# Optimization experiments

Measured on AMD Instinct MI355X. Metric: run time of the kernel, lower is better.

Reference implementation:

```python
import jax, jax.numpy as jnp
import numpy as np

BETA = 0.25
SCALE_NUM = 4  # len(latents_scale)


def setup_inputs() -> dict:
    key = jax.random.key(0)
    kz, ke = jax.random.split(key)
    z = jax.random.normal(kz, (8, 256, 32, 32), dtype=jnp.float32)
    emb_weight = jax.random.normal(ke, (16384, 256), dtype=jnp.float32) * 0.02
    return {"z": z, "emb_weight": emb_weight}


def reference(z, emb_weight):
    # z: [B, C, H, W] with C == vq_embed_dim and H == W (source reshapes with W twice)
    B, C, H, W = z.shape
    z_det = jax.lax.stop_gradient(z)

    # NOTE: in the source, `residual` is flattened ONCE before the scale loop and
    # never updated inside it, so every scale picks the same indices. We compute
    # the nearest-codebook assignment once (identical math, argmin of cdist is
    # invariant under sqrt, so squared distances suffice).
    residual = jnp.transpose(z_det, (0, 2, 3, 1)).reshape(-1, C)  # [N, D], N=B*H*W
    d2 = (jnp.sum(residual * residual, axis=1, keepdims=True)
          - 2.0 * residual @ emb_weight.T
          + jnp.sum(emb_weight * emb_weight, axis=1))  # [N, n_e]
    idx = jnp.argmin(d2, axis=1).reshape(B, W, W)  # [B, W, W]

    quantized = jnp.transpose(emb_weight[idx], (0, 3, 1, 2))  # [B, C, H, W]

    z_hat = jnp.zeros_like(z_det)
    loss = jnp.float32(0.0)
    for _ in range(SCALE_NUM):
        z_hat = z_hat + quantized
        loss = loss + BETA * jnp.mean((jax.lax.stop_gradient(z_hat) - z) ** 2) \
                    + jnp.mean((z_hat - z_det) ** 2)
    loss = loss / SCALE_NUM

    total_idx = jnp.concatenate([idx] * SCALE_NUM, axis=1)  # [B, SCALE_NUM*W, W]
    z_hat_out = z + jax.lax.stop_gradient(z_hat - z)  # straight-through
    return z_hat_out, loss, total_idx
```

## Files before the change

kernel.cpp:

```cpp
#include <hip/hip_runtime.h>

#define D      256
#define N_E    16384
#define NPTS   8192
#define ZOUT   2097152
#define MARGIN 2.0e-2f
#define STRIPS 4
#define ECH    17

typedef short bf16x8 __attribute__((ext_vector_type(8)));
typedef unsigned short us8 __attribute__((ext_vector_type(8)));
typedef float f32x16 __attribute__((ext_vector_type(16)));
typedef unsigned long long u64;

__device__ __forceinline__ unsigned short f2bf(float x) {
    unsigned int u = __float_as_uint(x);
    return (unsigned short)((u + 0x7FFFu + ((u >> 16) & 1u)) >> 16);
}
__device__ __forceinline__ float bf2f(unsigned short h) {
    return __uint_as_float((unsigned int)h << 16);
}
__device__ __forceinline__ void gl_lds16(const void* g, void* l) {
    __builtin_amdgcn_global_load_lds(
        (const __attribute__((address_space(1))) unsigned int*)g,
        (__attribute__((address_space(3))) unsigned int*)l, 16, 0, 0);
}

__global__ __launch_bounds__(256) void prep(
    const float* __restrict__ z, const float* __restrict__ emb,
    unsigned short* __restrict__ Zpk, float* __restrict__ Zf32,
    unsigned short* __restrict__ Epk, float* __restrict__ e2,
    float* __restrict__ loss) {
    __shared__ float sh[32];
    const int t = threadIdx.x;
    if (blockIdx.x == 0 && t == 0) loss[0] = 0.f;
    if (blockIdx.x < 256) {
        const int n0 = blockIdx.x * 32;
        const int p = t & 31, ks8 = t >> 5;
        const int n = n0 + p;
        const int b = n >> 10, hw = n & 1023;
        const float* zb = z + (size_t)b * 262144 + hw;
        const int k0 = ks8 * 32;
        float v[32];
        #pragma unroll
        for (int kk = 0; kk < 32; ++kk)
            v[kk] = zb[(size_t)(k0 + kk) * 1024];
        #pragma unroll
        for (int i = 0; i < 8; ++i) {
            float4 f = {v[i * 4], v[i * 4 + 1], v[i * 4 + 2], v[i * 4 + 3]};
            *(float4*)(Zf32 + (size_t)n * D + k0 + i * 4) = f;
        }
        const int g = n >> 5;
        #pragma unroll
        for (int i = 0; i < 4; ++i) {
            us8 hv;
            #pragma unroll
            for (int c = 0; c < 8; ++c) hv[c] = f2bf(-2.0f * v[i * 8 + c]);
            const int kabs = k0 + i * 8;
            const int ks = kabs >> 4;
            const int l = (n & 31) + ((kabs >> 3) & 1) * 32;
            *(us8*)(Zpk + ((size_t)(g * 16 + ks) * 64 + l) * 8) = hv;
        }
    } else {
        const int bi = blockIdx.x - 256;
        const int j0 = bi * 32;
        const int jj = j0 + (t >> 3), q = t & 7;
        const float* row = emb + (size_t)jj * D + q * 32;
        float v[32];
        float s = 0.f;
        #pragma unroll
        for (int i = 0; i < 8; ++i) {
            const float4 x = *(const float4*)(row + i * 4);
            v[i * 4] = x.x; v[i * 4 + 1] = x.y; v[i * 4 + 2] = x.z; v[i * 4 + 3] = x.w;
            s += x.x * x.x + x.y * x.y + x.z * x.z + x.w * x.w;
        }
        #pragma unroll
        for (int i = 0; i < 4; ++i) {
            us8 hv;
            #pragma unroll
            for (int c = 0; c < 8; ++c) hv[c] = f2bf(v[i * 8 + c]);
            const int kabs = q * 32 + i * 8;
            const int ks = kabs >> 4;
            const int l = (jj & 31) + ((kabs >> 3) & 1) * 32;
            *(us8*)(Epk + ((size_t)(bi * ECH + ks) * 64 + l) * 8) = hv;
        }
        s += __shfl_xor(s, 1);
        s += __shfl_xor(s, 2);
        s += __shfl_xor(s, 4);
        if (q == 0) { e2[jj] = s; sh[t >> 3] = s; }
        __syncthreads();
        if (t < 64) {
            us8 hv;
            #pragma unroll
            for (int c = 0; c < 8; ++c) hv[c] = 0;
            if (t < 32) {
                const float vv = sh[t];
                const unsigned short hi = f2bf(vv);
                hv[0] = hi;
                hv[1] = f2bf(vv - bf2f(hi));
            }
            *(us8*)(Epk + ((size_t)bi * ECH + 16) * 512 + t * 8) = hv;
        }
    }
}

__global__ __launch_bounds__(256, 1) void mfma_gemm(
    const unsigned short* __restrict__ Epk, const unsigned short* __restrict__ Zpk,
    float* __restrict__ tminv, u64* __restrict__ tmask) {
    __shared__ unsigned short Zbuf[64 * 512];

    const int tid = threadIdx.x, lane = tid & 63, wid = tid >> 6;
    const int c32 = lane & 31, l5 = lane >> 5;
    const int n0 = blockIdx.x * 128;
    const int cs0 = blockIdx.y * (STRIPS * 512);

    us8 puu;
    #pragma unroll
    for (int c = 0; c < 8; ++c) puu[c] = 0;
    if (l5 == 0) { puu[0] = 0x3F80; puu[1] = 0x3F80; }
    const bf16x8 pu = (bf16x8)puu;

    #pragma unroll
    for (int ks = 0; ks < 16; ++ks)
        gl_lds16(Zpk + ((size_t)((n0 >> 5) + wid) * 16 + ks) * 512 + lane * 8,
                 Zbuf + (wid * 16 + ks) * 512);
    __syncthreads();

    for (int s = 0; s < STRIPS; ++s) {
        const int cb = cs0 + s * 512 + wid * 128;
        const unsigned short* eb =
            Epk + ((size_t)(cb >> 5) * ECH) * 512 + lane * 8;
        const unsigned short* zb = Zbuf + lane * 8;

        f32x16 acc[4][4];
        const f32x16 z16 = {0.f};
        #pragma unroll
        for (int i = 0; i < 4; ++i)
            #pragma unroll
            for (int j = 0; j < 4; ++j) acc[i][j] = z16;

        bf16x8 eq0[4], eq1[4];
        #pragma unroll
        for (int f = 0; f < 4; ++f) {
            eq0[f] = *(const bf16x8*)(eb + (f * ECH + 0) * 512);
            eq1[f] = *(const bf16x8*)(eb + (f * ECH + 1) * 512);
        }
        bf16x8 pc[4], pn[4];
        #pragma unroll
        for (int j = 0; j < 4; ++j) pc[j] = *(const bf16x8*)(zb + (j * 16) * 512);

        #pragma unroll 2
        for (int ks = 0; ks < 16; ++ks) {
            bf16x8 ef[4];
            if ((ks & 1) == 0) {
                #pragma unroll
                for (int f = 0; f < 4; ++f) ef[f] = eq0[f];
            } else {
                #pragma unroll
                for (int f = 0; f < 4; ++f) ef[f] = eq1[f];
            }
            if (ks < 15) {
                if ((ks & 1) == 0) {
                    #pragma unroll
                    for (int f = 0; f < 4; ++f)
                        eq0[f] = *(const bf16x8*)(eb + (f * ECH + ks + 2) * 512);
                } else {
                    #pragma unroll
                    for (int f = 0; f < 4; ++f)
                        eq1[f] = *(const bf16x8*)(eb + (f * ECH + ks + 2) * 512);
                }
                #pragma unroll
                for (int j = 0; j < 4; ++j)
                    pn[j] = *(const bf16x8*)(zb + (j * 16 + ks + 1) * 512);
            }
            #pragma unroll
            for (int i = 0; i < 4; ++i)
                #pragma unroll
                for (int j = 0; j < 4; ++j)
                    acc[i][j] = __builtin_amdgcn_mfma_f32_32x32x16_bf16(
                        ef[i], pc[j], acc[i][j], 0, 0, 0);
            if (ks < 15) {
                #pragma unroll
                for (int j = 0; j < 4; ++j) pc[j] = pn[j];
            }
        }
        #pragma unroll
        for (int i = 0; i < 4; ++i)
            #pragma unroll
            for (int j = 0; j < 4; ++j)
                acc[i][j] = __builtin_amdgcn_mfma_f32_32x32x16_bf16(
                    eq0[i], pu, acc[i][j], 0, 0, 0);

        #pragma unroll
        for (int j = 0; j < 4; ++j) {
            #pragma unroll
            for (int gi = 0; gi < 2; ++gi) {
                float m = acc[2 * gi][j][0];
                #pragma unroll
                for (int r = 1; r < 16; ++r) m = fminf(m, acc[2 * gi][j][r]);
                #pragma unroll
                for (int r = 0; r < 16; ++r) m = fminf(m, acc[2 * gi + 1][j][r]);
                m = fminf(m, __shfl_xor(m, 32));
                const float th = m + MARGIN;
                unsigned mk[2];
                #pragma unroll
                for (int i = 0; i < 2; ++i) {
                    unsigned mm = 0;
                    #pragma unroll
                    for (int r = 0; r < 16; ++r) {
                        const int row = (r & 3) + 8 * (r >> 2) + 4 * l5;
                        mm |= (acc[2 * gi + i][j][r] <= th) ? (1u << row) : 0u;
                    }
                    mk[i] = mm | (unsigned)__shfl_xor((int)mm, 32);
                }
                if (l5 == 0) {
                    const size_t pt = (size_t)(n0 + j * 32 + c32);
                    const int g = (cb >> 6) + gi;
                    tminv[pt * 256 + g] = m;
                    tmask[pt * 256 + g] = ((u64)mk[1] << 32) | (u64)mk[0];
                }
            }
        }
    }
}

__global__ __launch_bounds__(1024) void rescore_quant(
    const float* __restrict__ tminv, const u64* __restrict__ tmask,
    const float* __restrict__ Zf32, const float* __restrict__ emb,
    const float* __restrict__ e2, const float* __restrict__ z,
    float* __restrict__ out, float* __restrict__ out_idx,
    float* __restrict__ loss) {
    __shared__ int idx_s[32];
    __shared__ float wsum[16];
    const int tid = threadIdx.x, lane = tid & 63, wd = tid >> 6;
    const int n0 = blockIdx.x * 32;
    const int b = n0 >> 10, hw0 = n0 & 1023;

    #pragma unroll 1
    for (int p = 0; p < 2; ++p) {
        const int lp = wd * 2 + p;
        const int n = n0 + lp;
        const float4 zr = *(const float4*)(Zf32 + (size_t)n * D + lane * 4);
        const float4 tv = *(const float4*)(tminv + (size_t)n * 256 + lane * 4);

        float m1 = fminf(fminf(tv.x, tv.y), fminf(tv.z, tv.w));
        #pragma unroll
        for (int st = 1; st < 64; st <<= 1) m1 = fminf(m1, __shfl_xor(m1, st));
        const float thresh = m1 + MARGIN;

        u64 best = ~0ull;
        const float tva[4] = {tv.x, tv.y, tv.z, tv.w};
        #pragma unroll
        for (int k = 0; k < 4; ++k) {
            u64 gm = __ballot(tva[k] <= thresh);
            while (gm) {
                const int bit = (int)__builtin_ctzll(gm);
                gm &= gm - 1;
                const int g = bit * 4 + k;
                u64 cm = tmask[(size_t)n * 256 + g];
                while (cm) {
                    const int r = (int)__builtin_ctzll(cm);
                    cm &= cm - 1;
                    const int c = g * 64 + r;
                    const float4 ev = *(const float4*)(emb + (size_t)c * D + lane * 4);
                    float s = zr.x * ev.x + zr.y * ev.y + zr.z * ev.z + zr.w * ev.w;
                    #pragma unroll
                    for (int st = 1; st < 64; st <<= 1) s += __shfl_xor(s, st);
                    const float d = e2[c] - 2.0f * s;
                    unsigned int u = __float_as_uint(d);
                    u = (u & 0x80000000u) ? ~u : (u | 0x80000000u);
                    const u64 key = ((u64)u << 32) | (unsigned int)c;
                    if (key < best) best = key;
                }
            }
        }
        if (lane == 0)
            idx_s[lp] = (int)(unsigned int)(best & 0xFFFFFFFFull);
    }
    __syncthreads();

    if (tid < 32) {
        const float fv = (float)idx_s[tid];
        #pragma unroll
        for (int sc = 0; sc < 4; ++sc)
            out_idx[b * 4096 + sc * 1024 + hw0 + tid] = fv;
    }
    const int hw_l = tid & 31, cg = tid >> 5;
    const int j = idx_s[hw_l];
    const float* er = emb + (size_t)j * D + cg * 8;
    const float4 q0 = *(const float4*)er;
    const float4 q1 = *(const float4*)(er + 4);
    const float qv[8] = {q0.x, q0.y, q0.z, q0.w, q1.x, q1.y, q1.z, q1.w};
    float e = 0.f;
    #pragma unroll
    for (int cc = 0; cc < 8; ++cc) {
        const int c = cg * 8 + cc;
        const size_t zi = (size_t)b * 262144 + (size_t)c * 1024 + hw0 + hw_l;
        const float zv = z[zi];
        const float q = qv[cc];
        const float zh = ((q + q) + q) + q;
        out[zi] = zv + (zh - zv);
        e += 30.0f * q * q - 20.0f * q * zv + 4.0f * zv * zv;
    }
    #pragma unroll
    for (int off = 32; off > 0; off >>= 1) e += __shfl_down(e, off);
    if (lane == 0) wsum[wd] = e;
    __syncthreads();
    if (tid == 0) {
        float s = 0.f;
        #pragma unroll
        for (int i = 0; i < 16; ++i) s += wsum[i];
        atomicAdd(loss, s * (0.3125f / 2097152.0f));
    }
}

extern "C" void kernel_launch(void* const* d_in, const int* in_sizes, int n_in,
                              void* d_out, int out_size, void* d_ws, size_t ws_size,
                              hipStream_t stream) {
    const float* z = (const float*)d_in[0];
    const float* emb = (const float*)d_in[1];
    float* out = (float*)d_out;

    unsigned short* Zpk = (unsigned short*)d_ws;
    unsigned short* Epk = Zpk + (size_t)NPTS * D;
    float* Zf32 = (float*)(Epk + (size_t)(N_E / 32) * ECH * 512);
    float* e2 = Zf32 + (size_t)NPTS * D;
    float* tminv = e2 + N_E;
    u64* tmask = (u64*)(tminv + (size_t)NPTS * 256);

    float* loss = out + ZOUT;
    float* out_idx = out + ZOUT + 1;

    prep<<<768, 256, 0, stream>>>(z, emb, Zpk, Zf32, Epk, e2, loss);
    mfma_gemm<<<dim3(NPTS / 128, N_E / (512 * STRIPS)), 256, 0, stream>>>(
        Epk, Zpk, tminv, tmask);
    rescore_quant<<<256, 1024, 0, stream>>>(tminv, tmask, Zf32, emb, e2, z,
                                            out, out_idx, loss);
}
```

Before: 178.9 us.

## Retile distance GEMM so all eight waves share one codebook strip per point slice

Result: slower. 194.5 us (+8.7%).

```diff
diff --git a/kernel.cpp b/kernel.cpp
--- a/kernel.cpp
+++ b/kernel.cpp
@@ -104,15 +104,15 @@
     }
 }
 
-__global__ __launch_bounds__(256, 1) void mfma_gemm(
+__global__ __launch_bounds__(512, 2) void mfma_gemm(
     const unsigned short* __restrict__ Epk, const unsigned short* __restrict__ Zpk,
     float* __restrict__ tminv, u64* __restrict__ tmask) {
-    __shared__ unsigned short Zbuf[64 * 512];
+    __shared__ unsigned short Zbuf[128 * 512];
 
     const int tid = threadIdx.x, lane = tid & 63, wid = tid >> 6;
     const int c32 = lane & 31, l5 = lane >> 5;
-    const int n0 = blockIdx.x * 128;
-    const int cs0 = blockIdx.y * (STRIPS * 512);
+    const int n0 = blockIdx.x * 256;
+    const int cs0 = blockIdx.y * (STRIPS * 256);
 
     us8 puu;
     #pragma unroll
@@ -121,106 +121,98 @@
     const bf16x8 pu = (bf16x8)puu;
 
     #pragma unroll
-    for (int ks = 0; ks < 16; ++ks)
-        gl_lds16(Zpk + ((size_t)((n0 >> 5) + wid) * 16 + ks) * 512 + lane * 8,
-                 Zbuf + (wid * 16 + ks) * 512);
+    for (int cc = 0; cc < 16; ++cc)
+        gl_lds16(Zpk + ((size_t)((n0 >> 5) + wid) * 16 + cc) * 512 + lane * 8,
+                 Zbuf + (wid * 16 + cc) * 512);
     __syncthreads();
 
+    const unsigned short* zb = Zbuf + (wid * 16) * 512 + lane * 8;
+
     for (int s = 0; s < STRIPS; ++s) {
-        const int cb = cs0 + s * 512 + wid * 128;
+        const int cb = cs0 + s * 256;
         const unsigned short* eb =
             Epk + ((size_t)(cb >> 5) * ECH) * 512 + lane * 8;
-        const unsigned short* zb = Zbuf + lane * 8;
-
-        f32x16 acc[4][4];
+
+        f32x16 acc[8];
         const f32x16 z16 = {0.f};
         #pragma unroll
-        for (int i = 0; i < 4; ++i)
-            #pragma unroll
-            for (int j = 0; j < 4; ++j) acc[i][j] = z16;
-
-        bf16x8 eq0[4], eq1[4];
-        #pragma unroll
-        for (int f = 0; f < 4; ++f) {
+        for (int i = 0; i < 8; ++i) acc[i] = z16;
+
+        bf16x8 eq0[8], eq1[8];
+        #pragma unroll
+        for (int f = 0; f < 8; ++f) {
             eq0[f] = *(const bf16x8*)(eb + (f * ECH + 0) * 512);
             eq1[f] = *(const bf16x8*)(eb + (f * ECH + 1) * 512);
         }
-        bf16x8 pc[4], pn[4];
-        #pragma unroll
-        for (int j = 0; j < 4; ++j) pc[j] = *(const bf16x8*)(zb + (j * 16) * 512);
-
-        #pragma unroll 2
-        for (int ks = 0; ks < 16; ++ks) {
-            bf16x8 ef[4];
-            if ((ks & 1) == 0) {
-                #pragma unroll
-                for (int f = 0; f < 4; ++f) ef[f] = eq0[f];
-            } else {
-                #pragma unroll
-                for (int f = 0; f < 4; ++f) ef[f] = eq1[f];
-            }
-            if (ks < 15) {
-                if ((ks & 1) == 0) {
+        bf16x8 pc = *(const bf16x8*)(zb);
+        bf16x8 pn;
+
+        #pragma unroll 1
+        for (int h = 0; h < 2; ++h) {
+            #pragma unroll 2
+            for (int k2 = 0; k2 < 8; ++k2) {
+                const int ks = h * 8 + k2;
+                bf16x8 ef[8];
+                if ((k2 & 1) == 0) {
                     #pragma unroll
-                    for (int f = 0; f < 4; ++f)
-                        eq0[f] = *(const bf16x8*)(eb + (f * ECH + ks + 2) * 512);
+                    for (int f = 0; f < 8; ++f) ef[f] = eq0[f];
                 } else {
                     #pragma unroll
-                    for (int f = 0; f < 4; ++f)
-                        eq1[f] = *(const bf16x8*)(eb + (f * ECH + ks + 2) * 512);
+                    for (int f = 0; f < 8; ++f) ef[f] = eq1[f];
+                }
+                if (ks < 15) {
+                    if ((k2 & 1) == 0) {
+                        #pragma unroll
+                        for (int f = 0; f < 8; ++f)
+                            eq0[f] = *(const bf16x8*)(eb + (f * ECH + ks + 2) * 512);
+                    } else {
+                        #pragma unroll
+                        for (int f = 0; f < 8; ++f)
+                            eq1[f] = *(const bf16x8*)(eb + (f * ECH + ks + 2) * 512);
+                    }
+                    pn = *(const bf16x8*)(zb + (ks + 1) * 512);
                 }
                 #pragma unroll
-                for (int j = 0; j < 4; ++j)
-                    pn[j] = *(const bf16x8*)(zb + (j * 16 + ks + 1) * 512);
-            }
-            #pragma unroll
-            for (int i = 0; i < 4; ++i)
+                for (int i = 0; i < 8; ++i)
+                    acc[i] = __builtin_amdgcn_mfma_f32_32x32x16_bf16(
+                        ef[i], pc, acc[i], 0, 0, 0);
+                if (ks < 15) pc = pn;
+            }
+            if (h == 0) __syncthreads();
+        }
+        #pragma unroll
+        for (int i = 0; i < 8; ++i)
+            acc[i] = __builtin_amdgcn_mfma_f32_32x32x16_bf16(
+                eq0[i], pu, acc[i], 0, 0, 0);
+
+        #pragma unroll
+        for (int gi = 0; gi < 4; ++gi) {
+            float m = acc[2 * gi][0];
+            #pragma unroll
+            for (int r = 1; r < 16; ++r) m = fminf(m, acc[2 * gi][r]);
+            #pragma unroll
+            for (int r = 0; r < 16; ++r) m = fminf(m, acc[2 * gi + 1][r]);
+            m = fminf(m, __shfl_xor(m, 32));
+            const float th = m + MARGIN;
+            unsigned mk[2];
+            #pragma unroll
+            for (int i = 0; i < 2; ++i) {
+                unsigned mm = 0;
                 #pragma unroll
-                for (int j = 0; j < 4; ++j)
-                    acc[i][j] = __builtin_amdgcn_mfma_f32_32x32x16_bf16(
-                        ef[i], pc[j], acc[i][j], 0, 0, 0);
-            if (ks < 15) {
-                #pragma unroll
-                for (int j = 0; j < 4; ++j) pc[j] = pn[j];
-            }
-        }
-        #pragma unroll
-        for (int i = 0; i < 4; ++i)
-            #pragma unroll
-            for (int j = 0; j < 4; ++j)
-                acc[i][j] = __builtin_amdgcn_mfma_f32_32x32x16_bf16(
-                    eq0[i], pu, acc[i][j], 0, 0, 0);
-
-        #pragma unroll
-        for (int j = 0; j < 4; ++j) {
-            #pragma unroll
-            for (int gi = 0; gi < 2; ++gi) {
-                float m = acc[2 * gi][j][0];
-                #pragma unroll
-                for (int r = 1; r < 16; ++r) m = fminf(m, acc[2 * gi][j][r]);
-                #pragma unroll
-                for (int r = 0; r < 16; ++r) m = fminf(m, acc[2 * gi + 1][j][r]);
-                m = fminf(m, __shfl_xor(m, 32));
-                const float th = m + MARGIN;
-                unsigned mk[2];
-                #pragma unroll
-                for (int i = 0; i < 2; ++i) {
-                    unsigned mm = 0;
-                    #pragma unroll
-                    for (int r = 0; r < 16; ++r) {
-                        const int row = (r & 3) + 8 * (r >> 2) + 4 * l5;
-                        mm |= (acc[2 * gi + i][j][r] <= th) ? (1u << row) : 0u;
-                    }
-                    mk[i] = mm | (unsigned)__shfl_xor((int)mm, 32);
+                for (int r = 0; r < 16; ++r) {
+                    const int row = (r & 3) + 8 * (r >> 2) + 4 * l5;
+                    mm |= (acc[2 * gi + i][r] <= th) ? (1u << row) : 0u;
                 }
-                if (l5 == 0) {
-                    const size_t pt = (size_t)(n0 + j * 32 + c32);
-                    const int g = (cb >> 6) + gi;
-                    tminv[pt * 256 + g] = m;
-                    tmask[pt * 256 + g] = ((u64)mk[1] << 32) | (u64)mk[0];
-                }
-            }
-        }
+                mk[i] = mm | (unsigned)__shfl_xor((int)mm, 32);
+            }
+            if (l5 == 0) {
+                const size_t pt = (size_t)(n0 + wid * 32 + c32);
+                const int g = (cb >> 6) + gi;
+                tminv[pt * 256 + g] = m;
+                tmask[pt * 256 + g] = ((u64)mk[1] << 32) | (u64)mk[0];
+            }
+        }
+        if (s < STRIPS - 1) __syncthreads();
     }
 }
 
@@ -332,7 +324,7 @@
     float* out_idx = out + ZOUT + 1;
 
     prep<<<768, 256, 0, stream>>>(z, emb, Zpk, Zf32, Epk, e2, loss);
-    mfma_gemm<<<dim3(NPTS / 128, N_E / (512 * STRIPS)), 256, 0, stream>>>(
+    mfma_gemm<<<dim3(NPTS / 256, N_E / (STRIPS * 256)), 512, 0, stream>>>(
         Epk, Zpk, tminv, tmask);
     rescore_quant<<<256, 1024, 0, stream>>>(tminv, tmask, Zf32, emb, e2, z,
                                             out, out_idx, loss);
```
